# Optimization experiments

Measured on AMD Instinct MI355X. Metric: run time of the kernel, lower is better.

The kernel has to match this reference:

```python
import jax, jax.numpy as jnp
import numpy as np

EPS_LN = 1e-6
EPS_STAT = 1e-10
EPS_BN = 1e-5


def _ln(x, g, b):
    mu = x.mean(-1, keepdims=True)
    var = x.var(-1, keepdims=True)
    return (x - mu) * jax.lax.rsqrt(var + EPS_LN) * g + b


def setup_inputs() -> dict:
    key = jax.random.key(0)
    ks = jax.random.split(key, 16)
    B, D, L, NB = 64, 256, 2048, 2
    H = 2 * D  # FFN inner dim
    s = 0.05   # small init scale for stability
    f32 = jnp.float32
    return {
        "x": jax.random.normal(ks[0], (B, D, L), f32),
        "wk": jax.random.normal(ks[1], (NB, 128, D), f32) * s,
        "wq": jax.random.normal(ks[2], (NB, 128, 2 * D), f32) * s,
        "fcq_w": jax.random.normal(ks[3], (NB, D, D), f32) * s,
        "fc_w": jax.random.normal(ks[4], (NB, D, 2 * D), f32) * s,
        "fc_b": jax.random.normal(ks[5], (NB, D), f32) * s,
        "att_ln_g": jnp.ones((NB, D), f32),
        "att_ln_b": jnp.zeros((NB, D), f32),
        "w1": jax.random.normal(ks[6], (NB, H, D), f32) * s,
        "b1": jax.random.normal(ks[7], (NB, H), f32) * s,
        "w2": jax.random.normal(ks[8], (NB, D, H), f32) * s,
        "b2": jax.random.normal(ks[9], (NB, D), f32) * s,
        "ffw_ln_g": jnp.ones((NB, D), f32),
        "ffw_ln_b": jnp.zeros((NB, D), f32),
    }


def reference(x, wk, wq, fcq_w, fc_w, fc_b, att_ln_g, att_ln_b,
              w1, b1, w2, b2, ffw_ln_g, ffw_ln_b):
    # x: (B, D, L)
    n_blocks = wk.shape[0]
    scale = 1.0 / np.sqrt(128.0)  # dim = k channel dim = 128
    v = x
    skip_sum = None
    for i in range(n_blocks):
        residual = v                                   # (B, D, L)
        vt = _ln(v.transpose(0, 2, 1), att_ln_g[i], att_ln_b[i])  # (B, L, D)
        k = jnp.einsum('bld,kd->blk', vt, wk[i])       # (B, L, 128)
        mu = vt.mean(axis=1, keepdims=True)            # (B, 1, D)
        sd = jnp.sqrt(jnp.clip(vt.var(axis=1, keepdims=True), EPS_STAT, None))
        q = jnp.einsum('bhe,ke->bhk',
                       jnp.concatenate([mu, sd], axis=2), wq[i])  # (B, 1, 128)
        scores = jnp.einsum('blk,bhk->bhl', k, q) * scale         # (B, 1, L)
        w = jax.nn.softmax(scores, axis=2)
        vdl = vt.transpose(0, 2, 1)                    # (B, D, L)
        att_mean = jnp.einsum('bdl,bhl->bdh', vdl, w)  # (B, D, 1)
        att_std = jnp.sqrt(jnp.clip(
            jnp.einsum('bdl,bhl->bdh', (vdl - att_mean) ** 2, w), EPS_STAT, None))
        skip = jnp.einsum('od,bdh->boh', fc_w[i],
                          jnp.concatenate([att_mean, att_std], axis=1)) \
               + fc_b[i][None, :, None]                # (B, D, 1)
        q_out = residual + jnp.einsum('od,bdh->boh', fcq_w[i], att_mean)  # (B, D, L)
        # PositionwiseFeedForward on (B, L, D)
        f_in = q_out.transpose(0, 2, 1)
        h = _ln(f_in, ffw_ln_g[i], ffw_ln_b[i])
        h1 = jax.nn.relu(jnp.einsum('bld,hd->blh', h, w1[i]) + b1[i])
        h2 = jnp.einsum('blh,dh->bld', h1, w2[i]) + b2[i]
        v = (h2 + f_in).transpose(0, 2, 1)             # (B, D, L)
        skip_sum = skip if skip_sum is None else skip_sum + skip
    # relu + BatchNorm1d (affine=False, training-mode batch stats)
    y = jax.nn.relu(skip_sum)                          # (B, D, 1)
    bm = y.mean(axis=(0, 2), keepdims=True)
    bv = y.var(axis=(0, 2), keepdims=True)
    return (y - bm) * jax.lax.rsqrt(bv + EPS_BN)
```

## Files before the change

### kernel.cpp

```cpp
#include <hip/hip_runtime.h>
#include <hip/hip_bf16.h>

#define DEV __device__ __forceinline__

constexpr int B = 64, D = 256, L = 2048, H = 512, KP = 128;
constexpr float EPS_LN = 1e-6f, EPS_STAT = 1e-10f, EPS_BN = 1e-5f;
constexpr float SCALE = 0.088388347648318447f;

typedef __attribute__((ext_vector_type(8))) short short8;
typedef __attribute__((ext_vector_type(4))) float float4_;

DEV unsigned short f2bf(float x) {
  unsigned u = __builtin_bit_cast(unsigned, x);
  u += 0x7fffu + ((u >> 16) & 1u);
  return (unsigned short)(u >> 16);
}

DEV unsigned pk2bf(float a, float b) {
  return (unsigned)f2bf(a) | ((unsigned)f2bf(b) << 16);
}

DEV float wred(float x) {
  #pragma unroll
  for (int o = 32; o > 0; o >>= 1) x += __shfl_down(x, o, 64);
  return x;
}
DEV float wredmax(float x) {
  #pragma unroll
  for (int o = 32; o > 0; o >>= 1) x = fmaxf(x, __shfl_down(x, o, 64));
  return x;
}

__global__ void k_convw(const float* __restrict__ w1, const float* __restrict__ w2,
                        unsigned short* __restrict__ w1b, unsigned short* __restrict__ w2b) {
  int n = H * D;
  for (int i = blockIdx.x * blockDim.x + threadIdx.x; i < n; i += gridDim.x * blockDim.x) {
    w1b[i] = f2bf(w1[i]);
    w2b[i] = f2bf(w2[i]);
  }
}

__global__ __launch_bounds__(512, 4) void k_pass1(
    const float* __restrict__ v, float* __restrict__ m, float* __restrict__ r,
    float* __restrict__ S1p, float* __restrict__ S2p) {
  __shared__ float part1[32 * 64], part2[32 * 64];
  __shared__ __align__(16) float mu_s[64], rs_s[64];

  int blk = blockIdx.x;
  int b = blk >> 5, tile = blk & 31, l0 = tile * 64;
  int tid = threadIdx.x;
  int lane4 = tid & 15, rg = tid >> 4;

  const float* vrow = v + ((size_t)b * D + rg * 8) * L + l0 + lane4 * 4;
  float4_ vv[8];
  float4_ s1 = {0.f, 0.f, 0.f, 0.f}, s2 = {0.f, 0.f, 0.f, 0.f};
  #pragma unroll
  for (int j = 0; j < 8; ++j) {
    float4_ x = *(const float4_*)&vrow[(size_t)j * L];
    vv[j] = x; s1 += x; s2 += x * x;
  }
  *(float4_*)&part1[rg * 64 + lane4 * 4] = s1;
  *(float4_*)&part2[rg * 64 + lane4 * 4] = s2;
  __syncthreads();
  if (tid < 64) {
    float a = 0.f, c = 0.f;
    #pragma unroll
    for (int q = 0; q < 32; ++q) { a += part1[q * 64 + tid]; c += part2[q * 64 + tid]; }
    float mu = a * (1.f / D);
    float var = c * (1.f / D) - mu * mu;
    float rsq = rsqrtf(var + EPS_LN);
    mu_s[tid] = mu; rs_s[tid] = rsq;
    m[b * L + l0 + tid] = mu;
    r[b * L + l0 + tid] = rsq;
  }
  __syncthreads();
  {
    float4_ mu4 = *(const float4_*)&mu_s[lane4 * 4];
    float4_ rs4 = *(const float4_*)&rs_s[lane4 * 4];
    size_t obase = ((size_t)b * 32 + tile) * D + rg * 8;
    #pragma unroll
    for (int j = 0; j < 8; ++j) {
      float4_ u = (vv[j] - mu4) * rs4;
      float a1 = u[0] + u[1] + u[2] + u[3];
      float a2 = u[0] * u[0] + u[1] * u[1] + u[2] * u[2] + u[3] * u[3];
      #pragma unroll
      for (int o = 1; o < 16; o <<= 1) {
        a1 += __shfl_xor(a1, o, 64);
        a2 += __shfl_xor(a2, o, 64);
      }
      if (lane4 == 0) { S1p[obase + j] = a1; S2p[obase + j] = a2; }
    }
  }
}

__global__ void k_qproj(const float* __restrict__ S1p, const float* __restrict__ S2p,
                        const float* __restrict__ g, const float* __restrict__ be,
                        const float* __restrict__ wq, const float* __restrict__ wk,
                        float* __restrict__ gw, float* __restrict__ Gg) {
  __shared__ float cat[2 * D];
  __shared__ float qs[KP];
  __shared__ float gsum[4];
  int b = blockIdx.x, t = threadIdx.x;
  {
    float s1 = 0.f, s2 = 0.f;
    for (int k = 0; k < 32; ++k) {
      s1 += S1p[((size_t)b * 32 + k) * D + t];
      s2 += S2p[((size_t)b * 32 + k) * D + t];
    }
    s1 *= (1.f / L); s2 *= (1.f / L);
    float gg = g[t];
    cat[t] = gg * s1 + be[t];
    float var = gg * gg * (s2 - s1 * s1);
    cat[D + t] = sqrtf(fmaxf(var, EPS_STAT));
  }
  __syncthreads();
  if (t < KP) {
    float s = 0.f;
    const float* wr = wq + t * 2 * D;
    for (int e = 0; e < 2 * D; ++e) s += cat[e] * wr[e];
    qs[t] = s;
  }
  __syncthreads();
  {
    float s = 0.f;
    for (int k = 0; k < KP; ++k) s += wk[k * D + t] * qs[k];
    float gwv = g[t] * SCALE * s;
    gw[b * D + t] = gwv;
    float gs = wred(gwv);
    if ((t & 63) == 0) gsum[t >> 6] = gs;
  }
  __syncthreads();
  if (t == 0) Gg[b] = gsum[0] + gsum[1] + gsum[2] + gsum[3];
}

__global__ __launch_bounds__(512) void k_scores(
    const float* __restrict__ v, const float* __restrict__ m,
    const float* __restrict__ r, const float* __restrict__ gw,
    const float* __restrict__ Gg, float* __restrict__ sc) {
  __shared__ float gws[D];
  __shared__ float sh[256];
  int blk = blockIdx.x;
  int b = blk >> 3, l0 = (blk & 7) * 256;
  int tid = threadIdx.x, lt = tid & 255, dh = tid >> 8;
  if (tid < D) gws[tid] = gw[b * D + tid];
  __syncthreads();
  int l = l0 + lt;
  const float* p = v + ((size_t)b * D + dh * 128) * L + l;
  float s = 0.f;
  #pragma unroll 8
  for (int d = 0; d < 128; ++d) s += p[(size_t)d * L] * gws[dh * 128 + d];
  if (dh == 1) sh[lt] = s;
  __syncthreads();
  if (dh == 0) {
    float tot = s + sh[lt];
    sc[b * L + l] = r[b * L + l] * (tot - m[b * L + l] * Gg[b]);
  }
}

__global__ __launch_bounds__(256) void k_redw(
    const float* __restrict__ v, const float* __restrict__ m, const float* __restrict__ r,
    const float* __restrict__ sc, float* __restrict__ A1, float* __restrict__ A2) {
  __shared__ float ws[L];
  __shared__ float ms[L], rs[L];
  __shared__ float red[4];
  int blk = blockIdx.x;
  int b = blk >> 4, dt = (blk & 15) * 16;
  int tid = threadIdx.x, wv = tid >> 6, lane = tid & 63;

  float xc[8];
  float mx = -1e30f;
  #pragma unroll
  for (int k = 0; k < 8; ++k) {
    float x = sc[b * L + tid + k * 256];
    xc[k] = x; mx = fmaxf(mx, x);
  }
  mx = wredmax(mx);
  if (lane == 0) red[wv] = mx;
  __syncthreads();
  mx = fmaxf(fmaxf(red[0], red[1]), fmaxf(red[2], red[3]));
  float sm = 0.f;
  #pragma unroll
  for (int k = 0; k < 8; ++k) { float e = __expf(xc[k] - mx); xc[k] = e; sm += e; }
  sm = wred(sm);
  __syncthreads();
  if (lane == 0) red[wv] = sm;
  __syncthreads();
  float inv = 1.f / (red[0] + red[1] + red[2] + red[3]);
  #pragma unroll
  for (int k = 0; k < 8; ++k) ws[tid + k * 256] = xc[k] * inv;
  for (int l = tid; l < L; l += 256) { ms[l] = m[b * L + l]; rs[l] = r[b * L + l]; }
  __syncthreads();

  for (int j = 0; j < 4; ++j) {
    int d = dt + wv * 4 + j;
    const float* row = v + ((size_t)b * D + d) * L;
    float a1 = 0.f, a2 = 0.f;
    #pragma unroll
    for (int k2 = 0; k2 < 8; ++k2) {
      int l = lane * 4 + k2 * 256;
      float4_ x4 = *(const float4_*)&row[l];
      #pragma unroll
      for (int i = 0; i < 4; ++i) {
        float u = (x4[i] - ms[l + i]) * rs[l + i];
        float w = ws[l + i];
        a1 += w * u; a2 += w * u * u;
      }
    }
    a1 = wred(a1); a2 = wred(a2);
    if (lane == 0) { A1[b * D + d] = a1; A2[b * D + d] = a2; }
  }
}

__global__ void k_skip(const float* __restrict__ A1, const float* __restrict__ A2,
                       const float* __restrict__ g, const float* __restrict__ be,
                       const float* __restrict__ fcw, const float* __restrict__ fcb,
                       const float* __restrict__ fcqw,
                       float* __restrict__ skip_i, float* __restrict__ fcq) {
  __shared__ float am[D], as_[D];
  int b = blockIdx.x, t = threadIdx.x;
  {
    float a1 = A1[b * D + t], a2 = A2[b * D + t], gg = g[t];
    am[t] = gg * a1 + be[t];
    float var = gg * gg * (a2 - a1 * a1);
    as_[t] = sqrtf(fmaxf(var, EPS_STAT));
  }
  __syncthreads();
  float s = fcb[t], fq = 0.f;
  const float* wr = fcw + t * 2 * D;
  const float* qr = fcqw + t * D;
  for (int d = 0; d < D; ++d) {
    s += wr[d] * am[d] + wr[D + d] * as_[d];
    fq += qr[d] * am[d];
  }
  skip_i[b * D + t] = s;
  fcq[b * D + t] = fq;
}

constexpr int MT = 64;

#define GEMM1_HALF(H0, ACC)                                                          \
  {                                                                                  \
    const unsigned short* wp0 = w1b + (size_t)((H0) + lr) * D + lq * 8;              \
    const unsigned short* wp1 = wp0 + 16 * D;                                        \
    short8 wr0[8], wr1[8];                                                           \
    _Pragma("unroll")                                                                \
    for (int kk = 0; kk < 8; ++kk) {                                                 \
      wr0[kk] = *(const short8*)(wp0 + kk * 32);                                     \
      wr1[kk] = *(const short8*)(wp1 + kk * 32);                                     \
    }                                                                                \
    int abase = lq * 512 + lr * 8;                                                   \
    _Pragma("unroll")                                                                \
    for (int kk = 0; kk < 8; ++kk) {                                                 \
      int nb = abase + kk * 2048;                                                    \
      short8 bf0 = *(const short8*)&us[nb];                                          \
      short8 bf1 = *(const short8*)&us[nb + 128];                                    \
      short8 bf2 = *(const short8*)&us[nb + 256];                                    \
      short8 bf3 = *(const short8*)&us[nb + 384];                                    \
      ACC[0][0] = __builtin_amdgcn_mfma_f32_16x16x32_bf16(wr0[kk], bf0, ACC[0][0],0,0,0);\
      ACC[0][1] = __builtin_amdgcn_mfma_f32_16x16x32_bf16(wr0[kk], bf1, ACC[0][1],0,0,0);\
      ACC[0][2] = __builtin_amdgcn_mfma_f32_16x16x32_bf16(wr0[kk], bf2, ACC[0][2],0,0,0);\
      ACC[0][3] = __builtin_amdgcn_mfma_f32_16x16x32_bf16(wr0[kk], bf3, ACC[0][3],0,0,0);\
      ACC[1][0] = __builtin_amdgcn_mfma_f32_16x16x32_bf16(wr1[kk], bf0, ACC[1][0],0,0,0);\
      ACC[1][1] = __builtin_amdgcn_mfma_f32_16x16x32_bf16(wr1[kk], bf1, ACC[1][1],0,0,0);\
      ACC[1][2] = __builtin_amdgcn_mfma_f32_16x16x32_bf16(wr1[kk], bf2, ACC[1][2],0,0,0);\
      ACC[1][3] = __builtin_amdgcn_mfma_f32_16x16x32_bf16(wr1[kk], bf3, ACC[1][3],0,0,0);\
    }                                                                                \
  }

#define H1_WRITE(H0, ACC)                                                            \
  {                                                                                  \
    _Pragma("unroll")                                                                \
    for (int mh = 0; mh < 2; ++mh) {                                                 \
      int hb = (H0) + mh * 16 + lq * 4;                                              \
      float b10 = b1[hb], b11 = b1[hb + 1], b12 = b1[hb + 2], b13 = b1[hb + 3];      \
      int grp = ((hb >> 3) + 32) & 63;                                               \
      int jh0 = hb & 7;                                                              \
      _Pragma("unroll")                                                              \
      for (int nt = 0; nt < 4; ++nt) {                                               \
        int tok = nt * 16 + lr;                                                      \
        uint2 pk;                                                                    \
        pk.x = pk2bf(fmaxf(ACC[mh][nt][0] + b10, 0.f),                               \
                     fmaxf(ACC[mh][nt][1] + b11, 0.f));                              \
        pk.y = pk2bf(fmaxf(ACC[mh][nt][2] + b12, 0.f),                               \
                     fmaxf(ACC[mh][nt][3] + b13, 0.f));                              \
        *(uint2*)&us[grp * 512 + tok * 8 + jh0] = pk;                                \
      }                                                                              \
    }                                                                                \
  }

#define GEMM2_HALF(M0, ACC2)                                                         \
  {                                                                                  \
    const unsigned short* wp = w2b + (size_t)((M0) + lr) * H + lq * 8;               \
    short8 wrg[16];                                                                  \
    _Pragma("unroll")                                                                \
    for (int kk = 0; kk < 16; ++kk) wrg[kk] = *(const short8*)(wp + kk * 32);        \
    _Pragma("unroll")                                                                \
    for (int kk = 0; kk < 16; ++kk) {                                                \
      int hb = ((kk * 4 + lq + 32) & 63) * 512 + lr * 8;                             \
      short8 hf0 = *(const short8*)&us[hb];                                          \
      short8 hf1 = *(const short8*)&us[hb + 128];                                    \
      short8 hf2 = *(const short8*)&us[hb + 256];                                    \
      short8 hf3 = *(const short8*)&us[hb + 384];                                    \
      ACC2[0] = __builtin_amdgcn_mfma_f32_16x16x32_bf16(wrg[kk], hf0, ACC2[0], 0, 0, 0);\
      ACC2[1] = __builtin_amdgcn_mfma_f32_16x16x32_bf16(wrg[kk], hf1, ACC2[1], 0, 0, 0);\
      ACC2[2] = __builtin_amdgcn_mfma_f32_16x16x32_bf16(wrg[kk], hf2, ACC2[2], 0, 0, 0);\
      ACC2[3] = __builtin_amdgcn_mfma_f32_16x16x32_bf16(wrg[kk], hf3, ACC2[3], 0, 0, 0);\
    }                                                                                \
  }

#define EPI_HALF(M0, ACC2)                                                           \
  {                                                                                  \
    _Pragma("unroll")                                                                \
    for (int i = 0; i < 4; ++i) {                                                    \
      int d = (M0) + lq * 4 + i;                                                     \
      float bb = b2_s[d] + fcq_s[d];                                                 \
      size_t rowoff = ((size_t)b * D + d) * L + l0;                                  \
      _Pragma("unroll")                                                              \
      for (int nt = 0; nt < 4; ++nt) {                                               \
        int tok = nt * 16 + lr;                                                      \
        dst[rowoff + tok] = ACC2[nt][i] + bb + src[rowoff + tok];                    \
      }                                                                              \
    }                                                                                \
  }

__global__ __launch_bounds__(512, 4) void k_ffn(
    const float* src, float* dst, const float* __restrict__ fcq,
    const unsigned short* __restrict__ w1b, const float* __restrict__ b1,
    const unsigned short* __restrict__ w2b, const float* __restrict__ b2,
    const float* __restrict__ g, const float* __restrict__ be) {
  __shared__ __align__(16) unsigned short us[32768];
  __shared__ float fcq_s[D], g_s[D], be_s[D], b2_s[D];
  __shared__ __align__(16) float mu_s[MT], rs_s[MT];
  float* part1 = (float*)us;
  float* part2 = (float*)(us + 4096);

  int blk = blockIdx.x;
  int b = blk >> 5;
  int l0 = (blk & 31) * MT;
  int tid = threadIdx.x;
  int lane4 = tid & 15, rg = tid >> 4;
  int wv = tid >> 6, lane = tid & 63, lr = lane & 15, lq = lane >> 4;

  if (tid < D) {
    fcq_s[tid] = fcq[b * D + tid];
    g_s[tid] = g[tid]; be_s[tid] = be[tid]; b2_s[tid] = b2[tid];
  }
  __syncthreads();

  const float* vrow = src + ((size_t)b * D + rg * 8) * L + l0 + lane4 * 4;
  float4_ vv[8];
  float4_ s1 = {0.f, 0.f, 0.f, 0.f}, s2 = {0.f, 0.f, 0.f, 0.f};
  #pragma unroll
  for (int j = 0; j < 8; ++j) {
    float4_ x = *(const float4_*)&vrow[(size_t)j * L];
    x = x + fcq_s[rg * 8 + j];
    vv[j] = x; s1 += x; s2 += x * x;
  }
  *(float4_*)&part1[rg * 64 + lane4 * 4] = s1;
  *(float4_*)&part2[rg * 64 + lane4 * 4] = s2;
  __syncthreads();
  if (tid < MT) {
    float a = 0.f, c = 0.f;
    #pragma unroll
    for (int q = 0; q < 32; ++q) { a += part1[q * 64 + tid]; c += part2[q * 64 + tid]; }
    float mu = a * (1.f / D);
    float var = c * (1.f / D) - mu * mu;
    mu_s[tid] = mu; rs_s[tid] = rsqrtf(var + EPS_LN);
  }
  __syncthreads();
  {
    float4_ mu4 = *(const float4_*)&mu_s[lane4 * 4];
    float4_ rs4 = *(const float4_*)&rs_s[lane4 * 4];
    #pragma unroll
    for (int c = 0; c < 4; ++c) {
      uint4 pw;
      unsigned* pp = &pw.x;
      #pragma unroll
      for (int jj = 0; jj < 4; ++jj) {
        int d0 = rg * 8 + jj * 2;
        pp[jj] = pk2bf((vv[jj * 2][c]     - mu4[c]) * rs4[c] * g_s[d0]     + be_s[d0],
                       (vv[jj * 2 + 1][c] - mu4[c]) * rs4[c] * g_s[d0 + 1] + be_s[d0 + 1]);
      }
      *(uint4*)&us[(rg * 64 + lane4 * 4 + c) * 8] = pw;
    }
  }
  __syncthreads();

  float4_ zero = {0.f, 0.f, 0.f, 0.f};

  {
    float4_ accA[2][4];
    #pragma unroll
    for (int i = 0; i < 2; ++i)
      #pragma unroll
      for (int j = 0; j < 4; ++j) accA[i][j] = zero;
    GEMM1_HALF(wv * 32, accA)
    H1_WRITE(wv * 32, accA)
  }
  {
    float4_ accB[2][4];
    #pragma unroll
    for (int i = 0; i < 2; ++i)
      #pragma unroll
      for (int j = 0; j < 4; ++j) accB[i][j] = zero;
    GEMM1_HALF(256 + wv * 32, accB)
    __syncthreads();
    H1_WRITE(256 + wv * 32, accB)
  }
  __syncthreads();

  {
    float4_ acc2[4];
    #pragma unroll
    for (int j = 0; j < 4; ++j) acc2[j] = zero;
    GEMM2_HALF(wv * 16, acc2)
    EPI_HALF(wv * 16, acc2)
  }
  {
    float4_ acc2[4];
    #pragma unroll
    for (int j = 0; j < 4; ++j) acc2[j] = zero;
    GEMM2_HALF(128 + wv * 16, acc2)
    EPI_HALF(128 + wv * 16, acc2)
  }
}

__global__ void k_bn(const float* __restrict__ s0, const float* __restrict__ s1,
                     float* __restrict__ out) {
  int d = threadIdx.x;
  float s = 0.f, q = 0.f;
  for (int b = 0; b < B; ++b) {
    float y = fmaxf(s0[b * D + d] + s1[b * D + d], 0.f);
    s += y; q += y * y;
  }
  float mu = s * (1.f / B);
  float var = q * (1.f / B) - mu * mu;
  float rs = rsqrtf(var + EPS_BN);
  for (int b = 0; b < B; ++b) {
    float y = fmaxf(s0[b * D + d] + s1[b * D + d], 0.f);
    out[b * D + d] = (y - mu) * rs;
  }
}

extern "C" void kernel_launch(void* const* d_in, const int* in_sizes, int n_in,
                              void* d_out, int out_size, void* d_ws, size_t ws_size,
                              hipStream_t stream) {
  const float* x    = (const float*)d_in[0];
  const float* wk   = (const float*)d_in[1];
  const float* wq   = (const float*)d_in[2];
  const float* fcqw = (const float*)d_in[3];
  const float* fcw  = (const float*)d_in[4];
  const float* fcb  = (const float*)d_in[5];
  const float* ag   = (const float*)d_in[6];
  const float* abt  = (const float*)d_in[7];
  const float* w1   = (const float*)d_in[8];
  const float* b1   = (const float*)d_in[9];
  const float* w2   = (const float*)d_in[10];
  const float* b2   = (const float*)d_in[11];
  const float* fg   = (const float*)d_in[12];
  const float* fb   = (const float*)d_in[13];
  float* out = (float*)d_out;

  char* p = (char*)d_ws;
  float* v_ws = (float*)p;  p += (size_t)B * D * L * 4;
  float* m    = (float*)p;  p += (size_t)B * L * 4;
  float* r    = (float*)p;  p += (size_t)B * L * 4;
  float* sc   = (float*)p;  p += (size_t)B * L * 4;
  float* S1p  = (float*)p;  p += (size_t)B * 32 * D * 4;
  float* S2p  = (float*)p;  p += (size_t)B * 32 * D * 4;
  float* gw   = (float*)p;  p += (size_t)B * D * 4;
  float* A1   = (float*)p;  p += (size_t)B * D * 4;
  float* A2   = (float*)p;  p += (size_t)B * D * 4;
  float* fcqv = (float*)p;  p += (size_t)B * D * 4;
  float* sk0  = (float*)p;  p += (size_t)B * D * 4;
  float* sk1  = (float*)p;  p += (size_t)B * D * 4;
  float* Gg   = (float*)p;  p += (size_t)B * 4;
  unsigned short* w1b = (unsigned short*)p; p += (size_t)H * D * 2;
  unsigned short* w2b = (unsigned short*)p; p += (size_t)D * H * 2;

  k_convw<<<256, 256, 0, stream>>>(w1, w2, w1b, w2b);

  for (int i = 0; i < 2; ++i) {
    const float* src = (i == 0) ? x : v_ws;
    k_pass1<<<B * 32, 512, 0, stream>>>(src, m, r, S1p, S2p);
    k_qproj<<<B, 256, 0, stream>>>(S1p, S2p, ag + i * D, abt + i * D,
                                   wq + (size_t)i * KP * 2 * D,
                                   wk + (size_t)i * KP * D, gw, Gg);
    k_scores<<<B * 8, 512, 0, stream>>>(src, m, r, gw, Gg, sc);
    k_redw<<<B * 16, 256, 0, stream>>>(src, m, r, sc, A1, A2);
    k_skip<<<B, 256, 0, stream>>>(A1, A2, ag + i * D, abt + i * D,
                                  fcw + (size_t)i * D * 2 * D, fcb + i * D,
                                  fcqw + (size_t)i * D * D,
                                  (i == 0) ? sk0 : sk1, fcqv);
    if (i == 0) {
      k_ffn<<<B * (L / MT), 512, 0, stream>>>(src, v_ws, fcqv,
                                              w1b, b1, w2b, b2, fg, fb);
    }
  }
  k_bn<<<1, 256, 0, stream>>>(sk0, sk1, out);
}
```

Measured before the change: 599.4 us.

## Fuse block-2 LayerNorm stats pass into FFN kernel epilogue

Fuses the second block's k_pass1 into the end of k_ffn. After writing its output tile, each FFN workgroup reads the tile back, computes per-token LN mean and rstd, and writes per-tile per-channel partial sums of the normalized values. This drops one full kernel launch and one full read of the 128MB activation from global memory. In exchange, the FFN kernel gets extra syncs, shuffles and register pressure, and the tile is re-read right after being written, which may or may not hit in cache.

```diff
diff --git a/kernel.cpp b/kernel.cpp
--- a/kernel.cpp
+++ b/kernel.cpp
@@ -327,7 +327,9 @@
     const float* src, float* dst, const float* __restrict__ fcq,
     const unsigned short* __restrict__ w1b, const float* __restrict__ b1,
     const unsigned short* __restrict__ w2b, const float* __restrict__ b2,
-    const float* __restrict__ g, const float* __restrict__ be) {
+    const float* __restrict__ g, const float* __restrict__ be,
+    float* __restrict__ m_o, float* __restrict__ r_o,
+    float* __restrict__ S1p, float* __restrict__ S2p) {
   __shared__ __align__(16) unsigned short us[32768];
   __shared__ float fcq_s[D], g_s[D], be_s[D], b2_s[D];
   __shared__ __align__(16) float mu_s[MT], rs_s[MT];
@@ -336,7 +338,8 @@
 
   int blk = blockIdx.x;
   int b = blk >> 5;
-  int l0 = (blk & 31) * MT;
+  int tile = blk & 31;
+  int l0 = tile * MT;
   int tid = threadIdx.x;
   int lane4 = tid & 15, rg = tid >> 4;
   int wv = tid >> 6, lane = tid & 63, lr = lane & 15, lq = lane >> 4;
@@ -348,27 +351,27 @@
   __syncthreads();
 
   const float* vrow = src + ((size_t)b * D + rg * 8) * L + l0 + lane4 * 4;
-  float4_ vv[8];
-  float4_ s1 = {0.f, 0.f, 0.f, 0.f}, s2 = {0.f, 0.f, 0.f, 0.f};
-  #pragma unroll
-  for (int j = 0; j < 8; ++j) {
-    float4_ x = *(const float4_*)&vrow[(size_t)j * L];
-    x = x + fcq_s[rg * 8 + j];
-    vv[j] = x; s1 += x; s2 += x * x;
-  }
-  *(float4_*)&part1[rg * 64 + lane4 * 4] = s1;
-  *(float4_*)&part2[rg * 64 + lane4 * 4] = s2;
-  __syncthreads();
-  if (tid < MT) {
-    float a = 0.f, c = 0.f;
-    #pragma unroll
-    for (int q = 0; q < 32; ++q) { a += part1[q * 64 + tid]; c += part2[q * 64 + tid]; }
-    float mu = a * (1.f / D);
-    float var = c * (1.f / D) - mu * mu;
-    mu_s[tid] = mu; rs_s[tid] = rsqrtf(var + EPS_LN);
-  }
-  __syncthreads();
-  {
+  {
+    float4_ vv[8];
+    float4_ s1 = {0.f, 0.f, 0.f, 0.f}, s2 = {0.f, 0.f, 0.f, 0.f};
+    #pragma unroll
+    for (int j = 0; j < 8; ++j) {
+      float4_ x = *(const float4_*)&vrow[(size_t)j * L];
+      x = x + fcq_s[rg * 8 + j];
+      vv[j] = x; s1 += x; s2 += x * x;
+    }
+    *(float4_*)&part1[rg * 64 + lane4 * 4] = s1;
+    *(float4_*)&part2[rg * 64 + lane4 * 4] = s2;
+    __syncthreads();
+    if (tid < MT) {
+      float a = 0.f, c = 0.f;
+      #pragma unroll
+      for (int q = 0; q < 32; ++q) { a += part1[q * 64 + tid]; c += part2[q * 64 + tid]; }
+      float mu = a * (1.f / D);
+      float var = c * (1.f / D) - mu * mu;
+      mu_s[tid] = mu; rs_s[tid] = rsqrtf(var + EPS_LN);
+    }
+    __syncthreads();
     float4_ mu4 = *(const float4_*)&mu_s[lane4 * 4];
     float4_ rs4 = *(const float4_*)&rs_s[lane4 * 4];
     #pragma unroll
@@ -422,6 +425,50 @@
     for (int j = 0; j < 4; ++j) acc2[j] = zero;
     GEMM2_HALF(128 + wv * 16, acc2)
     EPI_HALF(128 + wv * 16, acc2)
+  }
+
+  __syncthreads();
+  {
+    const float* drow = dst + ((size_t)b * D + rg * 8) * L + l0 + lane4 * 4;
+    float4_ vv[8];
+    float4_ s1 = {0.f, 0.f, 0.f, 0.f}, s2 = {0.f, 0.f, 0.f, 0.f};
+    #pragma unroll
+    for (int j = 0; j < 8; ++j) {
+      float4_ x = *(const float4_*)&drow[(size_t)j * L];
+      vv[j] = x; s1 += x; s2 += x * x;
+    }
+    *(float4_*)&part1[rg * 64 + lane4 * 4] = s1;
+    *(float4_*)&part2[rg * 64 + lane4 * 4] = s2;
+    __syncthreads();
+    if (tid < 64) {
+      float a = 0.f, c = 0.f;
+      #pragma unroll
+      for (int q = 0; q < 32; ++q) { a += part1[q * 64 + tid]; c += part2[q * 64 + tid]; }
+      float mu = a * (1.f / D);
+      float var = c * (1.f / D) - mu * mu;
+      float rsq = rsqrtf(var + EPS_LN);
+      mu_s[tid] = mu; rs_s[tid] = rsq;
+      m_o[b * L + l0 + tid] = mu;
+      r_o[b * L + l0 + tid] = rsq;
+    }
+    __syncthreads();
+    {
+      float4_ mu4 = *(const float4_*)&mu_s[lane4 * 4];
+      float4_ rs4 = *(const float4_*)&rs_s[lane4 * 4];
+      size_t obase = ((size_t)b * 32 + tile) * D + rg * 8;
+      #pragma unroll
+      for (int j = 0; j < 8; ++j) {
+        float4_ u = (vv[j] - mu4) * rs4;
+        float a1 = u[0] + u[1] + u[2] + u[3];
+        float a2 = u[0] * u[0] + u[1] * u[1] + u[2] * u[2] + u[3] * u[3];
+        #pragma unroll
+        for (int o = 1; o < 16; o <<= 1) {
+          a1 += __shfl_xor(a1, o, 64);
+          a2 += __shfl_xor(a2, o, 64);
+        }
+        if (lane4 == 0) { S1p[obase + j] = a1; S2p[obase + j] = a2; }
+      }
+    }
   }
 }
 
@@ -480,22 +527,22 @@
 
   k_convw<<<256, 256, 0, stream>>>(w1, w2, w1b, w2b);
 
-  for (int i = 0; i < 2; ++i) {
-    const float* src = (i == 0) ? x : v_ws;
-    k_pass1<<<B * 32, 512, 0, stream>>>(src, m, r, S1p, S2p);
-    k_qproj<<<B, 256, 0, stream>>>(S1p, S2p, ag + i * D, abt + i * D,
-                                   wq + (size_t)i * KP * 2 * D,
-                                   wk + (size_t)i * KP * D, gw, Gg);
-    k_scores<<<B * 8, 512, 0, stream>>>(src, m, r, gw, Gg, sc);
-    k_redw<<<B * 16, 256, 0, stream>>>(src, m, r, sc, A1, A2);
-    k_skip<<<B, 256, 0, stream>>>(A1, A2, ag + i * D, abt + i * D,
-                                  fcw + (size_t)i * D * 2 * D, fcb + i * D,
-                                  fcqw + (size_t)i * D * D,
-                                  (i == 0) ? sk0 : sk1, fcqv);
-    if (i == 0) {
-      k_ffn<<<B * (L / MT), 512, 0, stream>>>(src, v_ws, fcqv,
-                                              w1b, b1, w2b, b2, fg, fb);
-    }
-  }
+  k_pass1<<<B * 32, 512, 0, stream>>>(x, m, r, S1p, S2p);
+  k_qproj<<<B, 256, 0, stream>>>(S1p, S2p, ag, abt, wq, wk, gw, Gg);
+  k_scores<<<B * 8, 512, 0, stream>>>(x, m, r, gw, Gg, sc);
+  k_redw<<<B * 16, 256, 0, stream>>>(x, m, r, sc, A1, A2);
+  k_skip<<<B, 256, 0, stream>>>(A1, A2, ag, abt, fcw, fcb, fcqw, sk0, fcqv);
+  k_ffn<<<B * (L / MT), 512, 0, stream>>>(x, v_ws, fcqv, w1b, b1, w2b, b2,
+                                          fg, fb, m, r, S1p, S2p);
+
+  k_qproj<<<B, 256, 0, stream>>>(S1p, S2p, ag + D, abt + D,
+                                 wq + (size_t)KP * 2 * D, wk + (size_t)KP * D,
+                                 gw, Gg);
+  k_scores<<<B * 8, 512, 0, stream>>>(v_ws, m, r, gw, Gg, sc);
+  k_redw<<<B * 16, 256, 0, stream>>>(v_ws, m, r, sc, A1, A2);
+  k_skip<<<B, 256, 0, stream>>>(A1, A2, ag + D, abt + D,
+                                fcw + (size_t)D * 2 * D, fcb + D,
+                                fcqw + (size_t)D * D, sk1, fcqv);
+
   k_bn<<<1, 256, 0, stream>>>(sk0, sk1, out);
 }
```

New measurement: 598.3 us. About the same (-0.2%).
